# Kernel tuning notes

Hardware: AMD Instinct MI355X
Metric: run time of the kernel (lower is better)

The kernel has to match this reference:

```python
import jax, jax.numpy as jnp
import numpy as np

HEADS = 32
MAX_PERIOD = 10000.0
EPS = 1e-5


def layernorm(x, w, b):
    m = x.mean(-1, keepdims=True)
    v = ((x - m) ** 2).mean(-1, keepdims=True)
    return (x - m) * jax.lax.rsqrt(v + EPS) * w + b


def apply_rope(q, k, pos):
    # q, k: [B, T, H, D]; pos: [B, T] integer positions
    D = q.shape[-1]
    ds = D // 2
    inv_freq = 1.0 / (MAX_PERIOD ** (jnp.arange(ds, dtype=jnp.float32) / ds))
    ang = pos[..., None].astype(jnp.float32) * inv_freq          # [B, T, ds]
    cos = jnp.cos(ang)[:, :, None, :]                             # [B, T, 1, ds]
    sin = jnp.sin(ang)[:, :, None, :]

    def rot(t):
        tr, ti = t[..., 0::2], t[..., 1::2]
        out_r = tr * cos - ti * sin
        out_i = tr * sin + ti * cos
        return jnp.stack([out_r, out_i], axis=-1).reshape(t.shape)

    return rot(q), rot(k)


def setup_inputs() -> dict:
    key = jax.random.key(0)
    ks = jax.random.split(key, 8)
    B, T, C, F = 2, 1024, 2048, 8192
    H, D = HEADS, C // HEADS
    cap = 1024
    s = 0.02
    return {
        "x": jax.random.normal(ks[0], (B, T, C), jnp.float32),
        "cache": jnp.zeros((2, B, H, cap, D), jnp.float32),
        "in_proj_w": jax.random.normal(ks[1], (3 * C, C), jnp.float32) * s,
        "out_proj_w": jax.random.normal(ks[2], (C, C), jnp.float32) * s,
        "ln1_w": jnp.ones((C,), jnp.float32),
        "ln1_b": jnp.zeros((C,), jnp.float32),
        "ln2_w": jnp.ones((C,), jnp.float32),
        "ln2_b": jnp.zeros((C,), jnp.float32),
        "lin1_w": jax.random.normal(ks[3], (F, C), jnp.float32) * s,
        "lin2_w": jax.random.normal(ks[4], (C, F), jnp.float32) * s,
        "offset": jnp.zeros((B,), jnp.int64 if jax.config.jax_enable_x64 else jnp.int32),
        "end_offset": jnp.zeros((B,), jnp.int64 if jax.config.jax_enable_x64 else jnp.int32),
        "context": 512,
    }


def reference(x, cache, in_proj_w, out_proj_w, ln1_w, ln1_b, ln2_w, ln2_b,
              lin1_w, lin2_w, offset, end_offset, context):
    B, T, C = x.shape
    H = HEADS
    D = C // H
    cap = cache.shape[3]

    # ---- self-attention block ----
    h = layernorm(x, ln1_w, ln1_b)
    qkv = (h @ in_proj_w.T).reshape(B, T, 3, H, D)
    q, k, v = qkv[:, :, 0], qkv[:, :, 1], qkv[:, :, 2]           # [B, T, H, D]

    pos_q = offset[:, None] + jnp.arange(T)                       # [B, T]
    q, k = apply_rope(q, k, pos_q)

    q = q.transpose(0, 2, 1, 3)                                   # [B, H, T, D]
    k = k.transpose(0, 2, 1, 3)
    v = v.transpose(0, 2, 1, 3)

    # circular KV-cache update (functional version of `complete`)
    idx = (jnp.arange(T) + end_offset[:, None]) % cap             # [B, T]

    def upd(c, t, i):  # c: [H, cap, D], t: [H, T, D], i: [T]
        return c.at[:, i, :].set(t)

    keys = jax.vmap(upd)(cache[0], k, idx)                        # [B, H, cap, D]
    values = jax.vmap(upd)(cache[1], v, idx)

    slots = jnp.arange(cap)
    last = end_offset + T - 1                                     # [B]
    end_index = last % cap
    delta = slots[None, :] - end_index[:, None]                   # [B, cap]
    positions = jnp.where(delta <= 0, last[:, None] + delta,
                          last[:, None] + delta - cap)
    invalid = slots[None, :] >= (end_offset + T)[:, None]
    positions = jnp.where(invalid, -1, positions)                 # [B, cap]

    # sliding-window causal mask
    d = pos_q[:, :, None] - positions[:, None, :]                 # [B, T, cap]
    mask = (positions[:, None, :] >= 0) & (d >= 0) & (d < context)

    scale = 1.0 / jnp.sqrt(jnp.asarray(D, jnp.float32))
    scores = jnp.einsum('bhtd,bhsd->bhts', q, keys) * scale
    scores = jnp.where(mask[:, None], scores, jnp.asarray(-1e30, scores.dtype))
    attn = jax.nn.softmax(scores, axis=-1)
    o = jnp.einsum('bhts,bhsd->bhtd', attn, values)
    o = o.transpose(0, 2, 1, 3).reshape(B, T, C)
    x = x + o @ out_proj_w.T

    # ---- feed-forward block ----
    h2 = layernorm(x, ln2_w, ln2_b)
    ff = jax.nn.gelu(h2 @ lin1_w.T, approximate=False) @ lin2_w.T
    return x + ff
```

## Files before the change

kernel.cpp:

```cpp
#include <hip/hip_runtime.h>

typedef __attribute__((ext_vector_type(8))) short bf16x8;
typedef __attribute__((ext_vector_type(4))) float f32x4;
typedef __attribute__((ext_vector_type(8))) short short8v;
typedef __attribute__((ext_vector_type(4))) float float4v;

#define DEV static __device__ __forceinline__

DEV short f2bf(float f) {
  unsigned u = __builtin_bit_cast(unsigned, f);
  u = (u + 0x7fffu + ((u >> 16) & 1u)) >> 16;
  return (short)u;
}
DEV float bf2f(short s) {
  unsigned u = ((unsigned)(unsigned short)s) << 16;
  return __builtin_bit_cast(float, u);
}

DEV void gload_lds16(const void* g, void* l) {
  __builtin_amdgcn_global_load_lds((const __attribute__((address_space(1))) void*)g,
                                   (__attribute__((address_space(3))) void*)l, 16, 0, 0);
}

__global__ __launch_bounds__(256) void cvt_kernel(const float* __restrict__ src,
                                                  short* __restrict__ dst, int n8) {
  int i = blockIdx.x * 256 + threadIdx.x;
  const int stride = gridDim.x * 256;
  for (; i < n8; i += stride) {
    float4v a = ((const float4v*)src)[i * 2];
    float4v b = ((const float4v*)src)[i * 2 + 1];
    short8v o;
    o[0] = f2bf(a.x); o[1] = f2bf(a.y); o[2] = f2bf(a.z); o[3] = f2bf(a.w);
    o[4] = f2bf(b.x); o[5] = f2bf(b.y); o[6] = f2bf(b.z); o[7] = f2bf(b.w);
    ((short8v*)dst)[i] = o;
  }
}

__global__ __launch_bounds__(256) void ln_kernel(const float* __restrict__ x,
                                                 const float* __restrict__ w,
                                                 const float* __restrict__ b,
                                                 short* __restrict__ out) {
  const int C = 2048;
  const int row = blockIdx.x;
  const int tid = threadIdx.x;
  const float* xr = x + (size_t)row * C;
  float xv[8];
  *(float4v*)(xv) = *(const float4v*)(xr + tid * 8);
  *(float4v*)(xv + 4) = *(const float4v*)(xr + tid * 8 + 4);
  float s = 0.f, ss = 0.f;
#pragma unroll
  for (int i = 0; i < 8; ++i) { s += xv[i]; ss += xv[i] * xv[i]; }
#pragma unroll
  for (int d = 1; d < 64; d <<= 1) { s += __shfl_xor(s, d); ss += __shfl_xor(ss, d); }
  __shared__ float red[8];
  const int lane = tid & 63, wvv = tid >> 6;
  if (lane == 0) { red[wvv] = s; red[4 + wvv] = ss; }
  __syncthreads();
  s = red[0] + red[1] + red[2] + red[3];
  ss = red[4] + red[5] + red[6] + red[7];
  const float mean = s * (1.f / 2048.f);
  const float var = ss * (1.f / 2048.f) - mean * mean;
  const float rs = rsqrtf(var + 1e-5f);
  float wv8[8], bv8[8];
  *(float4v*)(wv8) = *(const float4v*)(w + tid * 8);
  *(float4v*)(wv8 + 4) = *(const float4v*)(w + tid * 8 + 4);
  *(float4v*)(bv8) = *(const float4v*)(b + tid * 8);
  *(float4v*)(bv8 + 4) = *(const float4v*)(b + tid * 8 + 4);
  short8v o;
#pragma unroll
  for (int i = 0; i < 8; ++i) o[i] = f2bf((xv[i] - mean) * rs * wv8[i] + bv8[i]);
  *(short8v*)(out + (size_t)row * C + tid * 8) = o;
}

template <int EPI>
__global__ __launch_bounds__(512, 2) void gemm256(const short* __restrict__ A,
                                                  const short* __restrict__ Bw,
                                                  void* __restrict__ C0, void* __restrict__ C1,
                                                  void* __restrict__ C2, void* __restrict__ C3,
                                                  int N, int K, int kChunk, int kTiles,
                                                  int rtx, int rty, int nrx) {
  extern __shared__ short smem[];
  const int tid = threadIdx.x;
  const int lane = tid & 63;
  const int wv = tid >> 6;
  const int wr = wv >> 2;
  const int wc = wv & 3;
  const int f2 = blockIdx.y * gridDim.x + blockIdx.x;
  const int xcd = f2 & 7, q = f2 >> 3;
  const int rx = xcd % nrx, ry = xcd / nrx;
  const int m0 = (ry * rty + q / rtx) * 256;
  const int n0 = (rx * rtx + q % rtx) * 256;
  const int kBegin = blockIdx.z * kChunk;

  const int l15 = lane & 15;
  const int lg = lane >> 4;

  const int fa0 = tid, fa1 = tid + 512;
  const int rA0 = fa0 >> 2, rA1 = fa1 >> 2;
  const int cA0 = (((fa0 & 3) ^ ((rA0 >> 1) & 3))) * 8;
  const int cA1 = (((fa1 & 3) ^ ((rA1 >> 1) & 3))) * 8;

  const short* Asrc0 = A + (size_t)(m0 + rA0) * K + kBegin + cA0;
  const short* Asrc1 = A + (size_t)(m0 + rA1) * K + kBegin + cA1;
  const short* Bsrc0 = Bw + (size_t)(n0 + rA0) * K + kBegin + cA0;
  const short* Bsrc1 = Bw + (size_t)(n0 + rA1) * K + kBegin + cA1;

  f32x4 acc[8][4] = {};

#define STAGE(t)                                                        \
  {                                                                     \
    short* dstb = smem + (((t) & 3) * 16384);                           \
    const size_t ko = (size_t)(t) * 32;                                 \
    gload_lds16(Asrc0 + ko, dstb + fa0 * 8);                            \
    gload_lds16(Asrc1 + ko, dstb + fa1 * 8);                            \
    gload_lds16(Bsrc0 + ko, dstb + 8192 + fa0 * 8);                     \
    gload_lds16(Bsrc1 + ko, dstb + 8192 + fa1 * 8);                     \
  }

  const int pre = kTiles < 3 ? kTiles : 3;
  for (int p = 0; p < pre; ++p) STAGE(p);

  for (int t = 0; t < kTiles; ++t) {
    const int rem = kTiles - 1 - t;
    if (rem >= 2) {
      asm volatile("s_waitcnt vmcnt(8)" ::: "memory");
    } else if (rem == 1) {
      asm volatile("s_waitcnt vmcnt(4)" ::: "memory");
    } else {
      asm volatile("s_waitcnt vmcnt(0)" ::: "memory");
    }
    __builtin_amdgcn_sched_barrier(0);
    __builtin_amdgcn_s_barrier();
    __builtin_amdgcn_sched_barrier(0);

    if (t + 3 < kTiles) STAGE(t + 3);

    const short* sa = smem + ((t & 3) * 16384);
    const short* sb = sa + 8192;
    bf16x8 af[8], bf[4];
#pragma unroll
    for (int m = 0; m < 8; ++m) {
      const int row = wr * 128 + m * 16 + l15;
      af[m] = *(const bf16x8*)(sa + row * 32 + ((lg ^ ((row >> 1) & 3)) * 8));
    }
#pragma unroll
    for (int n = 0; n < 4; ++n) {
      const int row = wc * 64 + n * 16 + l15;
      bf[n] = *(const bf16x8*)(sb + row * 32 + ((lg ^ ((row >> 1) & 3)) * 8));
    }
    __builtin_amdgcn_s_setprio(1);
#pragma unroll
    for (int m = 0; m < 8; ++m)
#pragma unroll
      for (int n = 0; n < 4; ++n)
        acc[m][n] = __builtin_amdgcn_mfma_f32_16x16x32_bf16(af[m], bf[n], acc[m][n], 0, 0, 0);
    __builtin_amdgcn_s_setprio(0);
  }
#undef STAGE

  void* Cout = blockIdx.z == 0 ? C0 : blockIdx.z == 1 ? C1 : blockIdx.z == 2 ? C2 : C3;
#pragma unroll
  for (int m = 0; m < 8; ++m) {
#pragma unroll
    for (int n = 0; n < 4; ++n) {
#pragma unroll
      for (int r = 0; r < 4; ++r) {
        const size_t idx =
            (size_t)(m0 + wr * 128 + m * 16 + lg * 4 + r) * N + (n0 + wc * 64 + n * 16 + l15);
        const float v = acc[m][n][r];
        if (EPI == 0) {
          ((short*)Cout)[idx] = f2bf(v);
        } else if (EPI == 2) {
          const float gl = 0.5f * v * (1.f + erff(v * 0.70710678118f));
          ((short*)Cout)[idx] = f2bf(gl);
        } else if (EPI == 3) {
          ((float*)Cout)[idx] = v;
        } else {
          if (blockIdx.z == 0)
            ((float*)Cout)[idx] = v;
          else
            ((short*)Cout)[idx] = f2bf(v);
        }
      }
    }
  }
}

__global__ __launch_bounds__(256) void reduce_k(float* __restrict__ dst,
                                                const float* __restrict__ resid,
                                                const float* __restrict__ p1,
                                                const float* __restrict__ p2,
                                                const float* __restrict__ p3,
                                                int ns, int n4) {
  int i = blockIdx.x * 256 + threadIdx.x;
  const int stride = gridDim.x * 256;
  for (; i < n4; i += stride) {
    float4v d = ((const float4v*)dst)[i];
    float4v r = ((const float4v*)resid)[i];
    float4v a = ((const float4v*)p1)[i];
    d.x += r.x + a.x; d.y += r.y + a.y; d.z += r.z + a.z; d.w += r.w + a.w;
    if (ns == 4) {
      float4v b = ((const float4v*)p2)[i];
      float4v c = ((const float4v*)p3)[i];
      d.x += b.x + c.x; d.y += b.y + c.y; d.z += b.z + c.z; d.w += b.w + c.w;
    }
    ((float4v*)dst)[i] = d;
  }
}

__global__ __launch_bounds__(256) void reduce_kb(float* __restrict__ dst,
                                                 const float* __restrict__ resid,
                                                 const short* __restrict__ p1,
                                                 int n8) {
  int i = blockIdx.x * 256 + threadIdx.x;
  const int stride = gridDim.x * 256;
  for (; i < n8; i += stride) {
    float4v d0 = ((const float4v*)dst)[i * 2];
    float4v d1 = ((const float4v*)dst)[i * 2 + 1];
    float4v r0 = ((const float4v*)resid)[i * 2];
    float4v r1 = ((const float4v*)resid)[i * 2 + 1];
    short8v p = ((const short8v*)p1)[i];
    d0.x += r0.x + bf2f(p[0]); d0.y += r0.y + bf2f(p[1]);
    d0.z += r0.z + bf2f(p[2]); d0.w += r0.w + bf2f(p[3]);
    d1.x += r1.x + bf2f(p[4]); d1.y += r1.y + bf2f(p[5]);
    d1.z += r1.z + bf2f(p[6]); d1.w += r1.w + bf2f(p[7]);
    ((float4v*)dst)[i * 2] = d0;
    ((float4v*)dst)[i * 2 + 1] = d1;
  }
}

__global__ __launch_bounds__(256) void rope_kernel(const short* __restrict__ qkv,
                                                   short* __restrict__ qo,
                                                   short* __restrict__ ko,
                                                   short* __restrict__ vo,
                                                   const int* __restrict__ offset) {
  const int T = 1024, H = 32;
  const int g = blockIdx.x * 256 + threadIdx.x;
  const int j = g & 31;
  const int h = (g >> 5) & 31;
  const int t = (g >> 10) & 1023;
  const int b = g >> 20;
  const size_t inb = (size_t)(b * T + t) * 6144 + h * 64 + 2 * j;
  const size_t outb = (size_t)((b * H + h) * T + t) * 64 + 2 * j;
  const int pos = offset[b] + t;
  const float ang = (float)pos * __builtin_exp2f(-13.287712379549449f * (float)j * (1.f / 32.f));
  float sn, c;
  __sincosf(ang, &sn, &c);
  const float qr = bf2f(qkv[inb]), qi = bf2f(qkv[inb + 1]);
  qo[outb] = f2bf(qr * c - qi * sn);
  qo[outb + 1] = f2bf(qr * sn + qi * c);
  const float kr = bf2f(qkv[inb + 2048]), ki = bf2f(qkv[inb + 2048 + 1]);
  ko[outb] = f2bf(kr * c - ki * sn);
  ko[outb + 1] = f2bf(kr * sn + ki * c);
  vo[outb] = qkv[inb + 4096];
  vo[outb + 1] = qkv[inb + 4096 + 1];
}

__global__ __launch_bounds__(256) void attn_kernel(const short* __restrict__ qb,
                                                   const short* __restrict__ kb,
                                                   const short* __restrict__ vb,
                                                   short* __restrict__ o,
                                                   const int* __restrict__ offset,
                                                   const int* __restrict__ end_offset,
                                                   const int* __restrict__ ctxp) {
  const int T = 1024;
  __shared__ short Ks[64 * 64];
  __shared__ short Vt[64 * 64];
  __shared__ short Ps[4][16 * 64];
  const int tid = threadIdx.x;
  const int lane = tid & 63;
  const int w = tid >> 6;
  const int blk = blockIdx.x;
  const int qt = blk & 15;
  const int bh = blk >> 4;
  const int b = bh >> 5;
  const int h = bh & 31;
  const int q0 = qt * 64;
  const int offq = offset[b];
  const int offk = end_offset[b];
  const int W = ctxp[0];
  const int odelta = offq - offk;

  const short* qp = qb + (size_t)bh * T * 64;
  const short* kp = kb + (size_t)bh * T * 64;
  const short* vp = vb + (size_t)bh * T * 64;

  const int l15 = lane & 15;
  const int lg = lane >> 4;

  bf16x8 qf[2];
  {
    const int qrow = q0 + w * 16 + l15;
    qf[0] = *(const bf16x8*)(qp + (size_t)qrow * 64 + lg * 8);
    qf[1] = *(const bf16x8*)(qp + (size_t)qrow * 64 + 32 + lg * 8);
  }

  f32x4 oacc[4] = {};
  float mrow[4] = {-1e30f, -1e30f, -1e30f, -1e30f};
  float ssum[4] = {0.f, 0.f, 0.f, 0.f};

  int kv_lo = q0 + odelta - (W - 1);
  if (kv_lo < 0) kv_lo = 0;
  int kv_hi = q0 + 63 + odelta;
  if (kv_hi > T - 1) kv_hi = T - 1;

  for (int t0 = (kv_lo & ~63); t0 <= kv_hi; t0 += 64) {
    __syncthreads();
#pragma unroll
    for (int j = 0; j < 2; ++j) {
      const int r0 = (j * 4 + w) * 8;
      gload_lds16(kp + (size_t)(t0 + r0 + (lane >> 3)) * 64 + (lane & 7) * 8, Ks + r0 * 64);
    }
#pragma unroll
    for (int j = 0; j < 2; ++j) {
      const int kv = (tid >> 3) + j * 32;
      const int d0 = (tid & 7) * 8;
      bf16x8 vv = *(const bf16x8*)(vp + (size_t)(t0 + kv) * 64 + d0);
#pragma unroll
      for (int i = 0; i < 8; ++i) Vt[(d0 + i) * 64 + kv] = vv[i];
    }
    __syncthreads();

    f32x4 s[4] = {};
#pragma unroll
    for (int n = 0; n < 4; ++n) {
      bf16x8 k0f = *(const bf16x8*)(Ks + (n * 16 + l15) * 64 + lg * 8);
      bf16x8 k1f = *(const bf16x8*)(Ks + (n * 16 + l15) * 64 + 32 + lg * 8);
      s[n] = __builtin_amdgcn_mfma_f32_16x16x32_bf16(qf[0], k0f, s[n], 0, 0, 0);
      s[n] = __builtin_amdgcn_mfma_f32_16x16x32_bf16(qf[1], k1f, s[n], 0, 0, 0);
    }

#pragma unroll
    for (int r = 0; r < 4; ++r) {
      const int tq = q0 + w * 16 + lg * 4 + r;
      float sv[4];
      float mx = -1e30f;
#pragma unroll
      for (int n = 0; n < 4; ++n) {
        const int tk = t0 + n * 16 + l15;
        const int dd = tq + odelta - tk;
        const bool valid = (dd >= 0) && (dd < W);
        sv[n] = valid ? s[n][r] * 0.125f : -1e30f;
        mx = fmaxf(mx, sv[n]);
      }
      mx = fmaxf(mx, __shfl_xor(mx, 1));
      mx = fmaxf(mx, __shfl_xor(mx, 2));
      mx = fmaxf(mx, __shfl_xor(mx, 4));
      mx = fmaxf(mx, __shfl_xor(mx, 8));
      const float mnew = fmaxf(mrow[r], mx);
      const float sf = __expf(mrow[r] - mnew);
      mrow[r] = mnew;
      float ls = 0.f;
#pragma unroll
      for (int n = 0; n < 4; ++n) {
        const float p = (sv[n] > -0.5e30f) ? __expf(sv[n] - mnew) : 0.f;
        ls += p;
        Ps[w][(lg * 4 + r) * 64 + n * 16 + l15] = f2bf(p);
      }
      ls += __shfl_xor(ls, 1);
      ls += __shfl_xor(ls, 2);
      ls += __shfl_xor(ls, 4);
      ls += __shfl_xor(ls, 8);
      ssum[r] = ssum[r] * sf + ls;
#pragma unroll
      for (int n = 0; n < 4; ++n) oacc[n][r] *= sf;
    }

#pragma unroll
    for (int ks = 0; ks < 2; ++ks) {
      bf16x8 pa = *(const bf16x8*)(&Ps[w][l15 * 64 + ks * 32 + lg * 8]);
#pragma unroll
      for (int n = 0; n < 4; ++n) {
        bf16x8 vf = *(const bf16x8*)(Vt + (n * 16 + l15) * 64 + ks * 32 + lg * 8);
        oacc[n] = __builtin_amdgcn_mfma_f32_16x16x32_bf16(pa, vf, oacc[n], 0, 0, 0);
      }
    }
  }

#pragma unroll
  for (int n = 0; n < 4; ++n) {
#pragma unroll
    for (int r = 0; r < 4; ++r) {
      const int tq = q0 + w * 16 + lg * 4 + r;
      const float val = oacc[n][r] / ssum[r];
      o[(size_t)(b * T + tq) * 2048 + h * 64 + n * 16 + l15] = f2bf(val);
    }
  }
}

extern "C" void kernel_launch(void* const* d_in, const int* in_sizes, int n_in,
                              void* d_out, int out_size, void* d_ws, size_t ws_size,
                              hipStream_t stream) {
  (void)in_sizes; (void)n_in; (void)out_size; (void)ws_size;
  const float* x          = (const float*)d_in[0];
  const float* in_proj_w  = (const float*)d_in[2];
  const float* out_proj_w = (const float*)d_in[3];
  const float* ln1_w      = (const float*)d_in[4];
  const float* ln1_b      = (const float*)d_in[5];
  const float* ln2_w      = (const float*)d_in[6];
  const float* ln2_b      = (const float*)d_in[7];
  const float* lin1_w     = (const float*)d_in[8];
  const float* lin2_w     = (const float*)d_in[9];
  const int* offset       = (const int*)d_in[10];
  const int* end_offset   = (const int*)d_in[11];
  const int* ctx          = (const int*)d_in[12];
  float* out = (float*)d_out;

  hipFuncSetAttribute((const void*)gemm256<0>, hipFuncAttributeMaxDynamicSharedMemorySize, 131072);
  hipFuncSetAttribute((const void*)gemm256<2>, hipFuncAttributeMaxDynamicSharedMemorySize, 131072);
  hipFuncSetAttribute((const void*)gemm256<3>, hipFuncAttributeMaxDynamicSharedMemorySize, 131072);
  hipFuncSetAttribute((const void*)gemm256<4>, hipFuncAttributeMaxDynamicSharedMemorySize, 131072);

  const size_t MiB = 1048576;
  char* ws = (char*)d_ws;
  float* x1    = (float*)(ws);
  short* hbuf  = (short*)(ws + 16 * MiB);
  short* qkv   = (short*)(ws + 24 * MiB);
  short* qr    = (short*)(ws + 48 * MiB);
  short* kr    = (short*)(ws + 56 * MiB);
  short* vr    = (short*)(ws + 64 * MiB);
  short* wb_in = (short*)(ws + 48 * MiB);
  short* wb_out= (short*)(ws + 24 * MiB);
  float* p1o   = (float*)(ws + 32 * MiB);
  float* p2o   = (float*)(ws + 48 * MiB);
  float* p3o   = (float*)(ws + 64 * MiB);
  short* g     = (short*)(ws + 24 * MiB);
  short* wb1   = (short*)(ws + 64 * MiB);
  short* wb2   = (short*)(ws + 56 * MiB);
  short* p1b   = (short*)(ws + 16 * MiB);

  ln_kernel<<<2048, 256, 0, stream>>>(x, ln1_w, ln1_b, hbuf);
  cvt_kernel<<<2048, 256, 0, stream>>>(in_proj_w, wb_in, 12582912 / 8);
  gemm256<0><<<dim3(24, 8, 1), 512, 131072, stream>>>(hbuf, wb_in, qkv, nullptr, nullptr, nullptr,
                                                      6144, 2048, 2048, 64, 6, 4, 4);
  rope_kernel<<<8192, 256, 0, stream>>>(qkv, qr, kr, vr, offset);
  attn_kernel<<<1024, 256, 0, stream>>>(qr, kr, vr, hbuf, offset, end_offset, ctx);
  cvt_kernel<<<2048, 256, 0, stream>>>(out_proj_w, wb_out, 4194304 / 8);
  gemm256<3><<<dim3(8, 8, 4), 512, 131072, stream>>>(hbuf, wb_out, x1, p1o, p2o, p3o,
                                                     2048, 2048, 512, 16, 4, 2, 2);
  reduce_k<<<1024, 256, 0, stream>>>(x1, x, p1o, p2o, p3o, 4, 1048576);
  ln_kernel<<<2048, 256, 0, stream>>>(x1, ln2_w, ln2_b, hbuf);
  cvt_kernel<<<2048, 256, 0, stream>>>(lin1_w, wb1, 16777216 / 8);
  gemm256<2><<<dim3(32, 8, 1), 512, 131072, stream>>>(hbuf, wb1, g, nullptr, nullptr, nullptr,
                                                      8192, 2048, 2048, 64, 8, 4, 4);
  cvt_kernel<<<2048, 256, 0, stream>>>(lin2_w, wb2, 16777216 / 8);
  gemm256<4><<<dim3(8, 8, 2), 512, 131072, stream>>>(g, wb2, out, p1b, nullptr, nullptr,
                                                     2048, 8192, 4096, 128, 4, 2, 2);
  reduce_kb<<<1024, 256, 0, stream>>>(out, x1, p1b, 524288);
}
```

Before: 493.0 us.

## Add 64-wide K-tile GEMM with phased prefetch for QKV and FFN1 projections

Introduces a new gemm8p kernel for the QKV and first FFN GEMMs. It uses 64-wide K tiles with a 128-byte XOR swizzle and double-buffered LDS. Global-to-LDS prefetch of the next tile is split across the four M-subphases of the MFMA loop, so loads overlap compute with finer-grained barriers. It also drops the XCD-aware block remapping and uses plain blockIdx tile mapping in both GEMM kernels. This may reduce L2 locality across XCDs and adds more barriers per K tile.

New measurement: 494.9 us. No clear change (+0.4%).

```diff
diff --git a/kernel.cpp b/kernel.cpp
--- a/kernel.cpp
+++ b/kernel.cpp
@@ -73,23 +73,141 @@
 }
 
 template <int EPI>
-__global__ __launch_bounds__(512, 2) void gemm256(const short* __restrict__ A,
-                                                  const short* __restrict__ Bw,
-                                                  void* __restrict__ C0, void* __restrict__ C1,
-                                                  void* __restrict__ C2, void* __restrict__ C3,
-                                                  int N, int K, int kChunk, int kTiles,
-                                                  int rtx, int rty, int nrx) {
+__global__ __launch_bounds__(512, 2) void gemm8p(const short* __restrict__ A,
+                                                 const short* __restrict__ Bw,
+                                                 void* __restrict__ Cout,
+                                                 int N, int K, int kTiles) {
   extern __shared__ short smem[];
   const int tid = threadIdx.x;
   const int lane = tid & 63;
   const int wv = tid >> 6;
   const int wr = wv >> 2;
   const int wc = wv & 3;
-  const int f2 = blockIdx.y * gridDim.x + blockIdx.x;
-  const int xcd = f2 & 7, q = f2 >> 3;
-  const int rx = xcd % nrx, ry = xcd / nrx;
-  const int m0 = (ry * rty + q / rtx) * 256;
-  const int n0 = (rx * rtx + q % rtx) * 256;
+  const int l15 = lane & 15;
+  const int lg = lane >> 4;
+
+  const int m0 = blockIdx.y * 256;
+  const int n0 = blockIdx.x * 256;
+
+  const short* Apan = A + (size_t)m0 * K;
+  const short* Bpan = Bw + (size_t)n0 * K;
+
+  f32x4 acc[8][4] = {};
+
+#define STAGE_H(panel, h1, ldsbase)                                                   \
+  {                                                                                   \
+    _Pragma("unroll") for (int qq = 0; qq < 2; ++qq) {                                \
+      const int f = tid + qq * 512;                                                   \
+      const int r = f >> 3;                                                           \
+      const int sl = f & 7;                                                           \
+      gload_lds16(panel + (size_t)((h1) * 128 + r) * K + kt64 + ((sl ^ (r & 7)) * 8), \
+                  (ldsbase) + f * 8);                                                 \
+    }                                                                                 \
+  }
+
+  {
+    const int kt64 = 0;
+    short* sA = smem;
+    short* sB = smem + 16384;
+    STAGE_H(Apan, 0, sA);
+    STAGE_H(Apan, 1, sA + 8192);
+    STAGE_H(Bpan, 0, sB);
+    STAGE_H(Bpan, 1, sB + 8192);
+  }
+
+  for (int kt = 0; kt < kTiles; ++kt) {
+    const short* sa = smem + (kt & 1) * 32768;
+    const short* sb = sa + 16384;
+    short* nsa = smem + ((kt + 1) & 1) * 32768;
+    short* nsb = nsa + 16384;
+    const int kt64 = (kt + 1) * 64;
+    bf16x8 bfr[4][2];
+
+#pragma unroll
+    for (int p = 0; p < 4; ++p) {
+      if (p == 0) {
+        asm volatile("s_waitcnt vmcnt(0)" ::: "memory");
+        __builtin_amdgcn_sched_barrier(0);
+      }
+      __builtin_amdgcn_s_barrier();
+      __builtin_amdgcn_sched_barrier(0);
+      if (p == 0 && kt + 1 < kTiles) {
+        STAGE_H(Apan, 0, nsa);
+        STAGE_H(Apan, 1, nsa + 8192);
+      }
+      if (p == 1 && kt + 1 < kTiles) {
+        STAGE_H(Bpan, 0, nsb);
+        STAGE_H(Bpan, 1, nsb + 8192);
+      }
+      if (p == 0) {
+#pragma unroll
+        for (int n = 0; n < 4; ++n)
+#pragma unroll
+          for (int kk = 0; kk < 2; ++kk) {
+            const int R = wc * 64 + n * 16 + l15;
+            bfr[n][kk] = *(const bf16x8*)(sb + R * 64 + (((kk * 4 + lg) ^ (R & 7)) * 8));
+          }
+      }
+      bf16x8 af[2][2];
+#pragma unroll
+      for (int mm = 0; mm < 2; ++mm)
+#pragma unroll
+        for (int kk = 0; kk < 2; ++kk) {
+          const int R = wr * 128 + (p * 2 + mm) * 16 + l15;
+          af[mm][kk] = *(const bf16x8*)(sa + R * 64 + (((kk * 4 + lg) ^ (R & 7)) * 8));
+        }
+      asm volatile("s_waitcnt lgkmcnt(0)" ::: "memory");
+      __builtin_amdgcn_sched_barrier(0);
+      __builtin_amdgcn_s_setprio(1);
+#pragma unroll
+      for (int mm = 0; mm < 2; ++mm)
+#pragma unroll
+        for (int n = 0; n < 4; ++n)
+#pragma unroll
+          for (int kk = 0; kk < 2; ++kk)
+            acc[p * 2 + mm][n] =
+                __builtin_amdgcn_mfma_f32_16x16x32_bf16(af[mm][kk], bfr[n][kk],
+                                                        acc[p * 2 + mm][n], 0, 0, 0);
+      __builtin_amdgcn_s_setprio(0);
+      __builtin_amdgcn_sched_barrier(0);
+    }
+  }
+#undef STAGE_H
+
+#pragma unroll
+  for (int m = 0; m < 8; ++m) {
+#pragma unroll
+    for (int n = 0; n < 4; ++n) {
+#pragma unroll
+      for (int r = 0; r < 4; ++r) {
+        const size_t idx =
+            (size_t)(m0 + wr * 128 + m * 16 + lg * 4 + r) * N + (n0 + wc * 64 + n * 16 + l15);
+        const float v = acc[m][n][r];
+        if (EPI == 0) {
+          ((short*)Cout)[idx] = f2bf(v);
+        } else {
+          const float gl = 0.5f * v * (1.f + erff(v * 0.70710678118f));
+          ((short*)Cout)[idx] = f2bf(gl);
+        }
+      }
+    }
+  }
+}
+
+template <int EPI>
+__global__ __launch_bounds__(512, 2) void gemm256(const short* __restrict__ A,
+                                                  const short* __restrict__ Bw,
+                                                  void* __restrict__ C0, void* __restrict__ C1,
+                                                  void* __restrict__ C2, void* __restrict__ C3,
+                                                  int N, int K, int kChunk, int kTiles) {
+  extern __shared__ short smem[];
+  const int tid = threadIdx.x;
+  const int lane = tid & 63;
+  const int wv = tid >> 6;
+  const int wr = wv >> 2;
+  const int wc = wv & 3;
+  const int m0 = blockIdx.y * 256;
+  const int n0 = blockIdx.x * 256;
   const int kBegin = blockIdx.z * kChunk;
 
   const int l15 = lane & 15;
@@ -168,12 +286,7 @@
         const size_t idx =
             (size_t)(m0 + wr * 128 + m * 16 + lg * 4 + r) * N + (n0 + wc * 64 + n * 16 + l15);
         const float v = acc[m][n][r];
-        if (EPI == 0) {
-          ((short*)Cout)[idx] = f2bf(v);
-        } else if (EPI == 2) {
-          const float gl = 0.5f * v * (1.f + erff(v * 0.70710678118f));
-          ((short*)Cout)[idx] = f2bf(gl);
-        } else if (EPI == 3) {
+        if (EPI == 3) {
           ((float*)Cout)[idx] = v;
         } else {
           if (blockIdx.z == 0)
@@ -406,8 +519,8 @@
   const int* ctx          = (const int*)d_in[12];
   float* out = (float*)d_out;
 
-  hipFuncSetAttribute((const void*)gemm256<0>, hipFuncAttributeMaxDynamicSharedMemorySize, 131072);
-  hipFuncSetAttribute((const void*)gemm256<2>, hipFuncAttributeMaxDynamicSharedMemorySize, 131072);
+  hipFuncSetAttribute((const void*)gemm8p<0>, hipFuncAttributeMaxDynamicSharedMemorySize, 131072);
+  hipFuncSetAttribute((const void*)gemm8p<2>, hipFuncAttributeMaxDynamicSharedMemorySize, 131072);
   hipFuncSetAttribute((const void*)gemm256<3>, hipFuncAttributeMaxDynamicSharedMemorySize, 131072);
   hipFuncSetAttribute((const void*)gemm256<4>, hipFuncAttributeMaxDynamicSharedMemorySize, 131072);
 
@@ -431,20 +544,18 @@
 
   ln_kernel<<<2048, 256, 0, stream>>>(x, ln1_w, ln1_b, hbuf);
   cvt_kernel<<<2048, 256, 0, stream>>>(in_proj_w, wb_in, 12582912 / 8);
-  gemm256<0><<<dim3(24, 8, 1), 512, 131072, stream>>>(hbuf, wb_in, qkv, nullptr, nullptr, nullptr,
-                                                      6144, 2048, 2048, 64, 6, 4, 4);
+  gemm8p<0><<<dim3(24, 8, 1), 512, 131072, stream>>>(hbuf, wb_in, qkv, 6144, 2048, 32);
   rope_kernel<<<8192, 256, 0, stream>>>(qkv, qr, kr, vr, offset);
   attn_kernel<<<1024, 256, 0, stream>>>(qr, kr, vr, hbuf, offset, end_offset, ctx);
   cvt_kernel<<<2048, 256, 0, stream>>>(out_proj_w, wb_out, 4194304 / 8);
   gemm256<3><<<dim3(8, 8, 4), 512, 131072, stream>>>(hbuf, wb_out, x1, p1o, p2o, p3o,
-                                                     2048, 2048, 512, 16, 4, 2, 2);
+                                                     2048, 2048, 512, 16);
   reduce_k<<<1024, 256, 0, stream>>>(x1, x, p1o, p2o, p3o, 4, 1048576);
   ln_kernel<<<2048, 256, 0, stream>>>(x1, ln2_w, ln2_b, hbuf);
   cvt_kernel<<<2048, 256, 0, stream>>>(lin1_w, wb1, 16777216 / 8);
-  gemm256<2><<<dim3(32, 8, 1), 512, 131072, stream>>>(hbuf, wb1, g, nullptr, nullptr, nullptr,
-                                                      8192, 2048, 2048, 64, 8, 4, 4);
+  gemm8p<2><<<dim3(32, 8, 1), 512, 131072, stream>>>(hbuf, wb1, g, 8192, 2048, 32);
   cvt_kernel<<<2048, 256, 0, stream>>>(lin2_w, wb2, 16777216 / 8);
   gemm256<4><<<dim3(8, 8, 2), 512, 131072, stream>>>(g, wb2, out, p1b, nullptr, nullptr,
-                                                     2048, 8192, 4096, 128, 4, 2, 2);
+                                                     2048, 8192, 4096, 128);
   reduce_kb<<<1024, 256, 0, stream>>>(out, x1, p1b, 524288);
 }
```

## Load B tiles through registers and drop XCD-aware block remapping in GEMM

Applied to the files above, without the earlier changes.

The GEMM pipeline changes from a 3-deep direct global-to-LDS prefetch for both operands. A is now prefetched two tiles ahead via LDS DMA, while B goes through registers one tile ahead and is written to LDS after the MFMA block. The XCD-aware tile remapping of block indices is also removed in favour of plain blockIdx mapping. This aims to overlap B's latency with compute differently, but it adds extra lgkmcnt waits and register pressure and gives up L2 locality per XCD.

After: 522.5 us. 6.0% more time.

```diff
diff --git a/kernel.cpp b/kernel.cpp
--- a/kernel.cpp
+++ b/kernel.cpp
@@ -77,19 +77,15 @@
                                                   const short* __restrict__ Bw,
                                                   void* __restrict__ C0, void* __restrict__ C1,
                                                   void* __restrict__ C2, void* __restrict__ C3,
-                                                  int N, int K, int kChunk, int kTiles,
-                                                  int rtx, int rty, int nrx) {
+                                                  int N, int K, int kChunk, int kTiles) {
   extern __shared__ short smem[];
   const int tid = threadIdx.x;
   const int lane = tid & 63;
   const int wv = tid >> 6;
   const int wr = wv >> 2;
   const int wc = wv & 3;
-  const int f2 = blockIdx.y * gridDim.x + blockIdx.x;
-  const int xcd = f2 & 7, q = f2 >> 3;
-  const int rx = xcd % nrx, ry = xcd / nrx;
-  const int m0 = (ry * rty + q / rtx) * 256;
-  const int n0 = (rx * rtx + q % rtx) * 256;
+  const int m0 = blockIdx.y * 256;
+  const int n0 = blockIdx.x * 256;
   const int kBegin = blockIdx.z * kChunk;
 
   const int l15 = lane & 15;
@@ -97,43 +93,54 @@
 
   const int fa0 = tid, fa1 = tid + 512;
   const int rA0 = fa0 >> 2, rA1 = fa1 >> 2;
-  const int cA0 = (((fa0 & 3) ^ ((rA0 >> 1) & 3))) * 8;
-  const int cA1 = (((fa1 & 3) ^ ((rA1 >> 1) & 3))) * 8;
-
-  const short* Asrc0 = A + (size_t)(m0 + rA0) * K + kBegin + cA0;
-  const short* Asrc1 = A + (size_t)(m0 + rA1) * K + kBegin + cA1;
-  const short* Bsrc0 = Bw + (size_t)(n0 + rA0) * K + kBegin + cA0;
-  const short* Bsrc1 = Bw + (size_t)(n0 + rA1) * K + kBegin + cA1;
+  const int sw0 = ((fa0 & 3) ^ ((rA0 >> 1) & 3)) * 8;
+  const int sw1 = ((fa1 & 3) ^ ((rA1 >> 1) & 3)) * 8;
+
+  const short* Asrc0 = A + (size_t)(m0 + rA0) * K + kBegin + sw0;
+  const short* Asrc1 = A + (size_t)(m0 + rA1) * K + kBegin + sw1;
+  const short* Bsrc0 = Bw + (size_t)(n0 + rA0) * K + kBegin + (fa0 & 3) * 8;
+  const short* Bsrc1 = Bw + (size_t)(n0 + rA1) * K + kBegin + (fa1 & 3) * 8;
+  const int wB0 = rA0 * 32 + sw0;
+  const int wB1 = rA1 * 32 + sw1;
 
   f32x4 acc[8][4] = {};
-
-#define STAGE(t)                                                        \
+  float4v br0, br1;
+
+#define A_STAGE(t)                                                      \
   {                                                                     \
-    short* dstb = smem + (((t) & 3) * 16384);                           \
+    short* d = smem + (((t) & 3) * 16384);                              \
     const size_t ko = (size_t)(t) * 32;                                 \
-    gload_lds16(Asrc0 + ko, dstb + fa0 * 8);                            \
-    gload_lds16(Asrc1 + ko, dstb + fa1 * 8);                            \
-    gload_lds16(Bsrc0 + ko, dstb + 8192 + fa0 * 8);                     \
-    gload_lds16(Bsrc1 + ko, dstb + 8192 + fa1 * 8);                     \
-  }
-
-  const int pre = kTiles < 3 ? kTiles : 3;
-  for (int p = 0; p < pre; ++p) STAGE(p);
+    gload_lds16(Asrc0 + ko, d + fa0 * 8);                               \
+    gload_lds16(Asrc1 + ko, d + fa1 * 8);                               \
+  }
+#define B_LOAD(t)                                                       \
+  {                                                                     \
+    const size_t ko = (size_t)(t) * 32;                                 \
+    br0 = *(const float4v*)(Bsrc0 + ko);                                \
+    br1 = *(const float4v*)(Bsrc1 + ko);                                \
+  }
+#define B_WRITE(t)                                                      \
+  {                                                                     \
+    short* d = smem + (((t) & 3) * 16384) + 8192;                       \
+    *(float4v*)(d + wB0) = br0;                                         \
+    *(float4v*)(d + wB1) = br1;                                         \
+  }
+
+  A_STAGE(0);
+  if (kTiles > 1) A_STAGE(1);
+  B_LOAD(0);
+  asm volatile("s_waitcnt vmcnt(0)" ::: "memory");
+  __builtin_amdgcn_sched_barrier(0);
+  B_WRITE(0);
 
   for (int t = 0; t < kTiles; ++t) {
-    const int rem = kTiles - 1 - t;
-    if (rem >= 2) {
-      asm volatile("s_waitcnt vmcnt(8)" ::: "memory");
-    } else if (rem == 1) {
-      asm volatile("s_waitcnt vmcnt(4)" ::: "memory");
-    } else {
-      asm volatile("s_waitcnt vmcnt(0)" ::: "memory");
-    }
+    asm volatile("s_waitcnt lgkmcnt(0)" ::: "memory");
     __builtin_amdgcn_sched_barrier(0);
     __builtin_amdgcn_s_barrier();
     __builtin_amdgcn_sched_barrier(0);
 
-    if (t + 3 < kTiles) STAGE(t + 3);
+    if (t + 1 < kTiles) B_LOAD(t + 1);
+    if (t + 2 < kTiles) A_STAGE(t + 2);
 
     const short* sa = smem + ((t & 3) * 16384);
     const short* sb = sa + 8192;
@@ -148,6 +155,8 @@
       const int row = wc * 64 + n * 16 + l15;
       bf[n] = *(const bf16x8*)(sb + row * 32 + ((lg ^ ((row >> 1) & 3)) * 8));
     }
+    asm volatile("s_waitcnt lgkmcnt(0)" ::: "memory");
+    __builtin_amdgcn_sched_barrier(0);
     __builtin_amdgcn_s_setprio(1);
 #pragma unroll
     for (int m = 0; m < 8; ++m)
@@ -155,8 +164,21 @@
       for (int n = 0; n < 4; ++n)
         acc[m][n] = __builtin_amdgcn_mfma_f32_16x16x32_bf16(af[m], bf[n], acc[m][n], 0, 0, 0);
     __builtin_amdgcn_s_setprio(0);
-  }
-#undef STAGE
+    __builtin_amdgcn_sched_barrier(0);
+
+    if (t + 1 < kTiles) {
+      if (t + 2 < kTiles) {
+        asm volatile("s_waitcnt vmcnt(2)" ::: "memory");
+      } else {
+        asm volatile("s_waitcnt vmcnt(0)" ::: "memory");
+      }
+      __builtin_amdgcn_sched_barrier(0);
+      B_WRITE(t + 1);
+    }
+  }
+#undef A_STAGE
+#undef B_LOAD
+#undef B_WRITE
 
   void* Cout = blockIdx.z == 0 ? C0 : blockIdx.z == 1 ? C1 : blockIdx.z == 2 ? C2 : C3;
 #pragma unroll
@@ -432,19 +454,19 @@
   ln_kernel<<<2048, 256, 0, stream>>>(x, ln1_w, ln1_b, hbuf);
   cvt_kernel<<<2048, 256, 0, stream>>>(in_proj_w, wb_in, 12582912 / 8);
   gemm256<0><<<dim3(24, 8, 1), 512, 131072, stream>>>(hbuf, wb_in, qkv, nullptr, nullptr, nullptr,
-                                                      6144, 2048, 2048, 64, 6, 4, 4);
+                                                      6144, 2048, 2048, 64);
   rope_kernel<<<8192, 256, 0, stream>>>(qkv, qr, kr, vr, offset);
   attn_kernel<<<1024, 256, 0, stream>>>(qr, kr, vr, hbuf, offset, end_offset, ctx);
   cvt_kernel<<<2048, 256, 0, stream>>>(out_proj_w, wb_out, 4194304 / 8);
   gemm256<3><<<dim3(8, 8, 4), 512, 131072, stream>>>(hbuf, wb_out, x1, p1o, p2o, p3o,
-                                                     2048, 2048, 512, 16, 4, 2, 2);
+                                                     2048, 2048, 512, 16);
   reduce_k<<<1024, 256, 0, stream>>>(x1, x, p1o, p2o, p3o, 4, 1048576);
   ln_kernel<<<2048, 256, 0, stream>>>(x1, ln2_w, ln2_b, hbuf);
   cvt_kernel<<<2048, 256, 0, stream>>>(lin1_w, wb1, 16777216 / 8);
   gemm256<2><<<dim3(32, 8, 1), 512, 131072, stream>>>(hbuf, wb1, g, nullptr, nullptr, nullptr,
-                                                      8192, 2048, 2048, 64, 8, 4, 4);
+                                                      8192, 2048, 2048, 64);
   cvt_kernel<<<2048, 256, 0, stream>>>(lin2_w, wb2, 16777216 / 8);
   gemm256<4><<<dim3(8, 8, 2), 512, 131072, stream>>>(g, wb2, out, p1b, nullptr, nullptr,
-                                                     2048, 8192, 4096, 128, 4, 2, 2);
+                                                     2048, 8192, 4096, 128);
   reduce_kb<<<1024, 256, 0, stream>>>(out, x1, p1b, 524288);
 }
```

## Interleave GEMM LDS reads, global prefetch and MFMA in four phases; drop XCD remap

Applied to the files above, without the earlier changes.

Splits the GEMM main loop into four phases. Each phase reads two A fragments from LDS, issues one of the four global-to-LDS prefetch loads, and runs eight MFMAs, so memory traffic is spread across the MFMA work and register pressure from eight A fragments drops. It adds three extra workgroup barriers per k-tile and explicit lgkmcnt waits. It also removes the XCD-aware block-to-tile remapping and uses plain blockIdx-based tile coordinates, which may hurt L2 locality across XCDs.

Result: slower. 512.7 us (+4.0%).

```diff
diff --git a/kernel.cpp b/kernel.cpp
--- a/kernel.cpp
+++ b/kernel.cpp
@@ -6,6 +6,7 @@
 typedef __attribute__((ext_vector_type(4))) float float4v;
 
 #define DEV static __device__ __forceinline__
+#define SB __builtin_amdgcn_sched_barrier(0)
 
 DEV short f2bf(float f) {
   unsigned u = __builtin_bit_cast(unsigned, f);
@@ -73,23 +74,19 @@
 }
 
 template <int EPI>
-__global__ __launch_bounds__(512, 2) void gemm256(const short* __restrict__ A,
+__global__ __launch_bounds__(512, 2) void gemm_fp(const short* __restrict__ A,
                                                   const short* __restrict__ Bw,
                                                   void* __restrict__ C0, void* __restrict__ C1,
                                                   void* __restrict__ C2, void* __restrict__ C3,
-                                                  int N, int K, int kChunk, int kTiles,
-                                                  int rtx, int rty, int nrx) {
+                                                  int N, int K, int kChunk, int kTiles) {
   extern __shared__ short smem[];
   const int tid = threadIdx.x;
   const int lane = tid & 63;
   const int wv = tid >> 6;
   const int wr = wv >> 2;
   const int wc = wv & 3;
-  const int f2 = blockIdx.y * gridDim.x + blockIdx.x;
-  const int xcd = f2 & 7, q = f2 >> 3;
-  const int rx = xcd % nrx, ry = xcd / nrx;
-  const int m0 = (ry * rty + q / rtx) * 256;
-  const int n0 = (rx * rtx + q % rtx) * 256;
+  const int m0 = blockIdx.y * 256;
+  const int n0 = blockIdx.x * 256;
   const int kBegin = blockIdx.z * kChunk;
 
   const int l15 = lane & 15;
@@ -97,8 +94,8 @@
 
   const int fa0 = tid, fa1 = tid + 512;
   const int rA0 = fa0 >> 2, rA1 = fa1 >> 2;
-  const int cA0 = (((fa0 & 3) ^ ((rA0 >> 1) & 3))) * 8;
-  const int cA1 = (((fa1 & 3) ^ ((rA1 >> 1) & 3))) * 8;
+  const int cA0 = ((fa0 & 3) ^ ((rA0 >> 1) & 3)) * 8;
+  const int cA1 = ((fa1 & 3) ^ ((rA1 >> 1) & 3)) * 8;
 
   const short* Asrc0 = A + (size_t)(m0 + rA0) * K + kBegin + cA0;
   const short* Asrc1 = A + (size_t)(m0 + rA1) * K + kBegin + cA1;
@@ -107,7 +104,7 @@
 
   f32x4 acc[8][4] = {};
 
-#define STAGE(t)                                                        \
+#define STAGE_FULL(t)                                                   \
   {                                                                     \
     short* dstb = smem + (((t) & 3) * 16384);                           \
     const size_t ko = (size_t)(t) * 32;                                 \
@@ -118,10 +115,27 @@
   }
 
   const int pre = kTiles < 3 ? kTiles : 3;
-  for (int p = 0; p < pre; ++p) STAGE(p);
+  for (int p = 0; p < pre; ++p) STAGE_FULL(p);
+
+#define RD_A(dst, mm)                                                    \
+  {                                                                      \
+    const int row = wr * 128 + (mm)*16 + l15;                            \
+    dst = *(const bf16x8*)(sa + row * 32 + ((lg ^ ((row >> 1) & 3)) * 8)); \
+  }
+#define MFMA2(mA, a0v, a1v)                                              \
+  _Pragma("unroll") for (int n = 0; n < 4; ++n) {                        \
+    acc[mA][n] = __builtin_amdgcn_mfma_f32_16x16x32_bf16(a0v, bfr[n], acc[mA][n], 0, 0, 0);      \
+    acc[mA + 1][n] = __builtin_amdgcn_mfma_f32_16x16x32_bf16(a1v, bfr[n], acc[mA + 1][n], 0, 0, 0); \
+  }
 
   for (int t = 0; t < kTiles; ++t) {
     const int rem = kTiles - 1 - t;
+    const short* sa = smem + ((t & 3) * 16384);
+    const short* sb = sa + 8192;
+    short* dstb = smem + (((t + 3) & 3) * 16384);
+    const size_t ko3 = (size_t)(t + 3) * 32;
+    const bool st = (t + 3 < kTiles);
+
     if (rem >= 2) {
       asm volatile("s_waitcnt vmcnt(8)" ::: "memory");
     } else if (rem == 1) {
@@ -129,34 +143,61 @@
     } else {
       asm volatile("s_waitcnt vmcnt(0)" ::: "memory");
     }
-    __builtin_amdgcn_sched_barrier(0);
+    SB;
     __builtin_amdgcn_s_barrier();
-    __builtin_amdgcn_sched_barrier(0);
-
-    if (t + 3 < kTiles) STAGE(t + 3);
-
-    const short* sa = smem + ((t & 3) * 16384);
-    const short* sb = sa + 8192;
-    bf16x8 af[8], bf[4];
-#pragma unroll
-    for (int m = 0; m < 8; ++m) {
-      const int row = wr * 128 + m * 16 + l15;
-      af[m] = *(const bf16x8*)(sa + row * 32 + ((lg ^ ((row >> 1) & 3)) * 8));
-    }
+    SB;
+    if (st) gload_lds16(Asrc0 + ko3, dstb + fa0 * 8);
+    bf16x8 bfr[4];
 #pragma unroll
     for (int n = 0; n < 4; ++n) {
       const int row = wc * 64 + n * 16 + l15;
-      bf[n] = *(const bf16x8*)(sb + row * 32 + ((lg ^ ((row >> 1) & 3)) * 8));
-    }
+      bfr[n] = *(const bf16x8*)(sb + row * 32 + ((lg ^ ((row >> 1) & 3)) * 8));
+    }
+    bf16x8 a0, a1;
+    RD_A(a0, 0); RD_A(a1, 1);
+    asm volatile("s_waitcnt lgkmcnt(0)" ::: "memory");
+    SB;
     __builtin_amdgcn_s_setprio(1);
-#pragma unroll
-    for (int m = 0; m < 8; ++m)
-#pragma unroll
-      for (int n = 0; n < 4; ++n)
-        acc[m][n] = __builtin_amdgcn_mfma_f32_16x16x32_bf16(af[m], bf[n], acc[m][n], 0, 0, 0);
+    MFMA2(0, a0, a1);
     __builtin_amdgcn_s_setprio(0);
-  }
-#undef STAGE
+    SB;
+
+    RD_A(a0, 2); RD_A(a1, 3);
+    __builtin_amdgcn_s_barrier();
+    SB;
+    if (st) gload_lds16(Asrc1 + ko3, dstb + fa1 * 8);
+    asm volatile("s_waitcnt lgkmcnt(0)" ::: "memory");
+    SB;
+    __builtin_amdgcn_s_setprio(1);
+    MFMA2(2, a0, a1);
+    __builtin_amdgcn_s_setprio(0);
+    SB;
+
+    RD_A(a0, 4); RD_A(a1, 5);
+    __builtin_amdgcn_s_barrier();
+    SB;
+    if (st) gload_lds16(Bsrc0 + ko3, dstb + 8192 + fa0 * 8);
+    asm volatile("s_waitcnt lgkmcnt(0)" ::: "memory");
+    SB;
+    __builtin_amdgcn_s_setprio(1);
+    MFMA2(4, a0, a1);
+    __builtin_amdgcn_s_setprio(0);
+    SB;
+
+    RD_A(a0, 6); RD_A(a1, 7);
+    __builtin_amdgcn_s_barrier();
+    SB;
+    if (st) gload_lds16(Bsrc1 + ko3, dstb + 8192 + fa1 * 8);
+    asm volatile("s_waitcnt lgkmcnt(0)" ::: "memory");
+    SB;
+    __builtin_amdgcn_s_setprio(1);
+    MFMA2(6, a0, a1);
+    __builtin_amdgcn_s_setprio(0);
+    SB;
+  }
+#undef STAGE_FULL
+#undef RD_A
+#undef MFMA2
 
   void* Cout = blockIdx.z == 0 ? C0 : blockIdx.z == 1 ? C1 : blockIdx.z == 2 ? C2 : C3;
 #pragma unroll
@@ -406,10 +447,10 @@
   const int* ctx          = (const int*)d_in[12];
   float* out = (float*)d_out;
 
-  hipFuncSetAttribute((const void*)gemm256<0>, hipFuncAttributeMaxDynamicSharedMemorySize, 131072);
-  hipFuncSetAttribute((const void*)gemm256<2>, hipFuncAttributeMaxDynamicSharedMemorySize, 131072);
-  hipFuncSetAttribute((const void*)gemm256<3>, hipFuncAttributeMaxDynamicSharedMemorySize, 131072);
-  hipFuncSetAttribute((const void*)gemm256<4>, hipFuncAttributeMaxDynamicSharedMemorySize, 131072);
+  hipFuncSetAttribute((const void*)gemm_fp<0>, hipFuncAttributeMaxDynamicSharedMemorySize, 131072);
+  hipFuncSetAttribute((const void*)gemm_fp<2>, hipFuncAttributeMaxDynamicSharedMemorySize, 131072);
+  hipFuncSetAttribute((const void*)gemm_fp<3>, hipFuncAttributeMaxDynamicSharedMemorySize, 131072);
+  hipFuncSetAttribute((const void*)gemm_fp<4>, hipFuncAttributeMaxDynamicSharedMemorySize, 131072);
 
   const size_t MiB = 1048576;
   char* ws = (char*)d_ws;
@@ -431,20 +472,20 @@
 
   ln_kernel<<<2048, 256, 0, stream>>>(x, ln1_w, ln1_b, hbuf);
   cvt_kernel<<<2048, 256, 0, stream>>>(in_proj_w, wb_in, 12582912 / 8);
-  gemm256<0><<<dim3(24, 8, 1), 512, 131072, stream>>>(hbuf, wb_in, qkv, nullptr, nullptr, nullptr,
-                                                      6144, 2048, 2048, 64, 6, 4, 4);
+  gemm_fp<0><<<dim3(24, 8, 1), 512, 131072, stream>>>(hbuf, wb_in, qkv, nullptr, nullptr, nullptr,
+                                                      6144, 2048, 2048, 64);
   rope_kernel<<<8192, 256, 0, stream>>>(qkv, qr, kr, vr, offset);
   attn_kernel<<<1024, 256, 0, stream>>>(qr, kr, vr, hbuf, offset, end_offset, ctx);
   cvt_kernel<<<2048, 256, 0, stream>>>(out_proj_w, wb_out, 4194304 / 8);
-  gemm256<3><<<dim3(8, 8, 4), 512, 131072, stream>>>(hbuf, wb_out, x1, p1o, p2o, p3o,
-                                                     2048, 2048, 512, 16, 4, 2, 2);
+  gemm_fp<3><<<dim3(8, 8, 4), 512, 131072, stream>>>(hbuf, wb_out, x1, p1o, p2o, p3o,
+                                                     2048, 2048, 512, 16);
   reduce_k<<<1024, 256, 0, stream>>>(x1, x, p1o, p2o, p3o, 4, 1048576);
   ln_kernel<<<2048, 256, 0, stream>>>(x1, ln2_w, ln2_b, hbuf);
   cvt_kernel<<<2048, 256, 0, stream>>>(lin1_w, wb1, 16777216 / 8);
-  gemm256<2><<<dim3(32, 8, 1), 512, 131072, stream>>>(hbuf, wb1, g, nullptr, nullptr, nullptr,
-                                                      8192, 2048, 2048, 64, 8, 4, 4);
+  gemm_fp<2><<<dim3(32, 8, 1), 512, 131072, stream>>>(hbuf, wb1, g, nullptr, nullptr, nullptr,
+                                                      8192, 2048, 2048, 64);
   cvt_kernel<<<2048, 256, 0, stream>>>(lin2_w, wb2, 16777216 / 8);
-  gemm256<4><<<dim3(8, 8, 2), 512, 131072, stream>>>(g, wb2, out, p1b, nullptr, nullptr,
-                                                     2048, 8192, 4096, 128, 4, 2, 2);
+  gemm_fp<4><<<dim3(8, 8, 2), 512, 131072, stream>>>(g, wb2, out, p1b, nullptr, nullptr,
+                                                     2048, 8192, 4096, 128);
   reduce_kb<<<1024, 256, 0, stream>>>(out, x1, p1b, 524288);
 }
```
